# Optimization experiments

Hardware: AMD Instinct MI355X
Metric: run time of the kernel (lower is better)

The kernel has to match this reference:

```python
import jax, jax.numpy as jnp
import numpy as np

UNITS = 256
BATCH = 256


def _make_sizes():
    rng = np.random.default_rng(0)
    nclasses = rng.integers(2, 16, size=BATCH).astype(np.int32)
    nfeature = rng.integers(50, 201, size=BATCH).astype(np.int32)
    return nclasses, nfeature


def setup_inputs() -> dict:
    key = jax.random.key(0)
    nclasses, nfeature = _make_sizes()
    total = int((nclasses.astype(np.int64) * nfeature).sum())
    x = jax.random.normal(key, (total, UNITS), dtype=jnp.float32)
    return {
        "x": x,
        "nclasses": jnp.asarray(nclasses),
        "nfeature": jnp.asarray(nfeature),
    }


def reference(x, nclasses, nfeature):
    # sizes[i] = nclasses[i] * nfeature[i]; segment i covers rows [start_i, start_i + sizes_i)
    sizes = (nclasses * nfeature).astype(jnp.int32)          # [B]
    num_segments = sizes.shape[0]
    ends = jnp.cumsum(sizes)                                  # [B]
    # segment id of each row: first segment whose end exceeds the row index
    seg_ids = jnp.searchsorted(ends, jnp.arange(x.shape[0]), side="right")
    sums = jax.ops.segment_sum(x, seg_ids, num_segments=num_segments)  # [B, units]
    return sums / sizes[:, None].astype(x.dtype)              # per-segment mean
```

## Files before the change

kernel.cpp:

```cpp
#include <hip/hip_runtime.h>

#define UNITS 256
#define BATCH 256

typedef float fx4 __attribute__((ext_vector_type(4)));

__global__ __launch_bounds__(256) void k_zero(float* __restrict__ out) {
    const int i = (blockIdx.x * 256 + threadIdx.x) << 2;
    *reinterpret_cast<fx4*>(out + i) = fx4{0.f, 0.f, 0.f, 0.f};
}

__global__ __launch_bounds__(256) void k_accum(const float* __restrict__ x,
                                               const int* __restrict__ nclasses,
                                               const int* __restrict__ nfeature,
                                               float* __restrict__ out,
                                               int total_rows, int lo, int nE4) {
    __shared__ int   s_ends[BATCH];
    __shared__ float s_inv[BATCH];
    __shared__ fx4   s_red[3][64];
    const int t  = threadIdx.x;
    const int ln = t & 63;
    const int rl = t >> 6;

    {
        const int sz = nclasses[t] * nfeature[t];
        s_inv[t]  = 1.0f / (float)sz;
        s_ends[t] = sz;
    }
    __syncthreads();
    #pragma unroll
    for (int off = 1; off < BATCH; off <<= 1) {
        int v   = s_ends[t];
        int add = (t >= off) ? s_ends[t - off] : 0;
        __syncthreads();
        s_ends[t] = v + add;
        __syncthreads();
    }

    const int b    = blockIdx.x;
    const int hi   = lo + 4;
    const int r0   = (b < nE4) ? b * hi : nE4 * hi + (b - nE4) * lo;
    const int sz   = (b < nE4) ? hi : lo;
    const int rend = min(r0 + sz, total_rows);
    if (r0 >= rend) return;

    int slo = 0, shi = BATCH;
    while (slo < shi) {
        int mid = (slo + shi) >> 1;
        if (s_ends[mid] > r0) shi = mid; else slo = mid + 1;
    }
    int seg = slo;

    const int c = ln << 2;
    int r = r0 + rl;
    const float* p = x + (size_t)r * UNITS + c;

    for (;;) {
        const int stop = min(s_ends[seg], rend);
        int cnt = (stop - r + 3) >> 2;
        if (cnt < 0) cnt = 0;
        r += cnt << 2;

        fx4 acc = {0.f, 0.f, 0.f, 0.f};
        int k = 0;
        for (; k + 8 <= cnt; k += 8) {
            fx4 v0 = __builtin_nontemporal_load((const fx4*)(p));
            fx4 v1 = __builtin_nontemporal_load((const fx4*)(p + 4  * UNITS));
            fx4 v2 = __builtin_nontemporal_load((const fx4*)(p + 8  * UNITS));
            fx4 v3 = __builtin_nontemporal_load((const fx4*)(p + 12 * UNITS));
            fx4 v4 = __builtin_nontemporal_load((const fx4*)(p + 16 * UNITS));
            fx4 v5 = __builtin_nontemporal_load((const fx4*)(p + 20 * UNITS));
            fx4 v6 = __builtin_nontemporal_load((const fx4*)(p + 24 * UNITS));
            fx4 v7 = __builtin_nontemporal_load((const fx4*)(p + 28 * UNITS));
            p += 32 * UNITS;
            acc += ((v0 + v1) + (v2 + v3)) + ((v4 + v5) + (v6 + v7));
        }
        for (; k < cnt; ++k) {
            fx4 v = __builtin_nontemporal_load((const fx4*)(p));
            p += 4 * UNITS;
            acc += v;
        }

        if (rl) s_red[rl - 1][ln] = acc;
        __syncthreads();
        if (rl == 0) {
            acc += s_red[0][ln];
            acc += s_red[1][ln];
            acc += s_red[2][ln];
            const float s = s_inv[seg];
            float* o = out + seg * UNITS + c;
            unsafeAtomicAdd(o + 0, acc.x * s);
            unsafeAtomicAdd(o + 1, acc.y * s);
            unsafeAtomicAdd(o + 2, acc.z * s);
            unsafeAtomicAdd(o + 3, acc.w * s);
        }
        if (s_ends[seg] >= rend) break;
        ++seg;
        __syncthreads();
    }
}

extern "C" void kernel_launch(void* const* d_in, const int* in_sizes, int n_in,
                              void* d_out, int out_size, void* d_ws, size_t ws_size,
                              hipStream_t stream) {
    const float* x        = (const float*)d_in[0];
    const int*   nclasses = (const int*)d_in[1];
    const int*   nfeature = (const int*)d_in[2];
    float*       out      = (float*)d_out;

    const int total_rows = in_sizes[0] / UNITS;

    const int q   = total_rows >> 11;
    const int lo  = q & ~3;
    const int E   = total_rows - (lo << 11);
    const int nE4 = (E + 3) >> 2;

    k_zero<<<64, 256, 0, stream>>>(out);
    k_accum<<<2048, 256, 0, stream>>>(x, nclasses, nfeature, out,
                                      total_rows, lo, nE4);
}
```

Before: 58.13 us.

## Use wave-shuffle prefix scan and spread segment atomics across all threads

```diff
diff --git a/kernel.cpp b/kernel.cpp
--- a/kernel.cpp
+++ b/kernel.cpp
@@ -17,31 +17,36 @@
                                                int total_rows, int lo, int nE4) {
     __shared__ int   s_ends[BATCH];
     __shared__ float s_inv[BATCH];
-    __shared__ fx4   s_red[3][64];
+    __shared__ int   s_wsum[4];
+    __shared__ float s_red[4][64][4];
     const int t  = threadIdx.x;
     const int ln = t & 63;
     const int rl = t >> 6;
 
     {
         const int sz = nclasses[t] * nfeature[t];
-        s_inv[t]  = 1.0f / (float)sz;
-        s_ends[t] = sz;
-    }
-    __syncthreads();
-    #pragma unroll
-    for (int off = 1; off < BATCH; off <<= 1) {
-        int v   = s_ends[t];
-        int add = (t >= off) ? s_ends[t - off] : 0;
+        s_inv[t] = 1.0f / (float)sz;
+        int v = sz;
+        #pragma unroll
+        for (int off = 1; off < 64; off <<= 1) {
+            int u = __shfl_up(v, off, 64);
+            if (ln >= off) v += u;
+        }
+        if (ln == 63) s_wsum[rl] = v;
         __syncthreads();
-        s_ends[t] = v + add;
+        int base = 0;
+        #pragma unroll
+        for (int w = 0; w < 3; ++w)
+            if (w < rl) base += s_wsum[w];
+        s_ends[t] = v + base;
         __syncthreads();
     }
 
     const int b    = blockIdx.x;
     const int hi   = lo + 4;
     const int r0   = (b < nE4) ? b * hi : nE4 * hi + (b - nE4) * lo;
-    const int sz   = (b < nE4) ? hi : lo;
-    const int rend = min(r0 + sz, total_rows);
+    const int csz  = (b < nE4) ? hi : lo;
+    const int rend = min(r0 + csz, total_rows);
     if (r0 >= rend) return;
 
     int slo = 0, shi = BATCH;
@@ -54,6 +59,7 @@
     const int c = ln << 2;
     int r = r0 + rl;
     const float* p = x + (size_t)r * UNITS + c;
+    fx4 acc = {0.f, 0.f, 0.f, 0.f};
 
     for (;;) {
         const int stop = min(s_ends[seg], rend);
@@ -61,41 +67,32 @@
         if (cnt < 0) cnt = 0;
         r += cnt << 2;
 
-        fx4 acc = {0.f, 0.f, 0.f, 0.f};
         int k = 0;
-        for (; k + 8 <= cnt; k += 8) {
-            fx4 v0 = __builtin_nontemporal_load((const fx4*)(p));
-            fx4 v1 = __builtin_nontemporal_load((const fx4*)(p + 4  * UNITS));
-            fx4 v2 = __builtin_nontemporal_load((const fx4*)(p + 8  * UNITS));
-            fx4 v3 = __builtin_nontemporal_load((const fx4*)(p + 12 * UNITS));
-            fx4 v4 = __builtin_nontemporal_load((const fx4*)(p + 16 * UNITS));
-            fx4 v5 = __builtin_nontemporal_load((const fx4*)(p + 20 * UNITS));
-            fx4 v6 = __builtin_nontemporal_load((const fx4*)(p + 24 * UNITS));
-            fx4 v7 = __builtin_nontemporal_load((const fx4*)(p + 28 * UNITS));
-            p += 32 * UNITS;
-            acc += ((v0 + v1) + (v2 + v3)) + ((v4 + v5) + (v6 + v7));
+        for (; k + 4 <= cnt; k += 4) {
+            fx4 v0 = *(const fx4*)(p);
+            fx4 v1 = *(const fx4*)(p + 4  * UNITS);
+            fx4 v2 = *(const fx4*)(p + 8  * UNITS);
+            fx4 v3 = *(const fx4*)(p + 12 * UNITS);
+            p += 16 * UNITS;
+            acc += (v0 + v1) + (v2 + v3);
         }
         for (; k < cnt; ++k) {
-            fx4 v = __builtin_nontemporal_load((const fx4*)(p));
+            fx4 v = *(const fx4*)(p);
             p += 4 * UNITS;
             acc += v;
         }
 
-        if (rl) s_red[rl - 1][ln] = acc;
+        *reinterpret_cast<fx4*>(&s_red[rl][ln][0]) = acc;
         __syncthreads();
-        if (rl == 0) {
-            acc += s_red[0][ln];
-            acc += s_red[1][ln];
-            acc += s_red[2][ln];
-            const float s = s_inv[seg];
-            float* o = out + seg * UNITS + c;
-            unsafeAtomicAdd(o + 0, acc.x * s);
-            unsafeAtomicAdd(o + 1, acc.y * s);
-            unsafeAtomicAdd(o + 2, acc.z * s);
-            unsafeAtomicAdd(o + 3, acc.w * s);
+        {
+            const int q  = t >> 2, e = t & 3;
+            const float vsum = s_red[0][q][e] + s_red[1][q][e]
+                             + s_red[2][q][e] + s_red[3][q][e];
+            unsafeAtomicAdd(out + seg * UNITS + t, vsum * s_inv[seg]);
         }
         if (s_ends[seg] >= rend) break;
         ++seg;
+        acc = fx4{0.f, 0.f, 0.f, 0.f};
         __syncthreads();
     }
 }
```

After: 53.91 us (median of 2 runs). -7.3%, faster.
